# Performance work log

Measured on AMD Instinct MI355X. Metric: run time of the kernel, lower is better.

Reference implementation:

```python
import jax, jax.numpy as jnp
import numpy as np

N = 100000
E = 1600000
F_IN = 128
H = 256
C = 40
BN_EPS = 1e-5


def setup_inputs() -> dict:
    key = jax.random.key(0)
    ks = jax.random.split(key, 16)
    x = jax.random.normal(ks[0], (N, F_IN), dtype=jnp.float32)
    edge_index = jax.random.randint(ks[1], (2, E), 0, N, dtype=jnp.int64)
    # pre layer
    pre_w = jax.random.normal(ks[2], (H, F_IN), dtype=jnp.float32) * (1.0 / np.sqrt(F_IN))
    pre_b = jnp.zeros((H,), jnp.float32)
    # batchnorm params stacked [5, 4, H]: gamma, beta, running_mean, running_var
    gamma = jnp.ones((5, H), jnp.float32)
    beta = jnp.zeros((5, H), jnp.float32)
    rmean = jax.random.normal(ks[3], (5, H), dtype=jnp.float32) * 0.1
    rvar = jax.random.uniform(ks[4], (5, H), dtype=jnp.float32) * 0.5 + 0.5
    bn_params = jnp.stack([gamma, beta, rmean, rvar], axis=1)  # [5,4,H]
    # 3 SAGEConv layers: lin_l (neighbor, with bias), lin_r (root, no bias)
    s = 1.0 / np.sqrt(H)
    lin_l_w = jax.random.normal(ks[5], (3, H, H), dtype=jnp.float32) * s
    lin_l_b = jnp.zeros((3, H), jnp.float32)
    lin_r_w = jax.random.normal(ks[6], (3, H, H), dtype=jnp.float32) * s
    # post layers
    post1_w = jax.random.normal(ks[7], (H, H), dtype=jnp.float32) * s
    post1_b = jnp.zeros((H,), jnp.float32)
    post2_w = jax.random.normal(ks[8], (C, H), dtype=jnp.float32) * s
    post2_b = jnp.zeros((C,), jnp.float32)
    return {
        "x": x, "edge_index": edge_index,
        "pre_w": pre_w, "pre_b": pre_b, "bn_params": bn_params,
        "lin_l_w": lin_l_w, "lin_l_b": lin_l_b, "lin_r_w": lin_r_w,
        "post1_w": post1_w, "post1_b": post1_b,
        "post2_w": post2_w, "post2_b": post2_b,
    }


def _bn(x, p):
    # eval-mode BatchNorm1d with running stats; p: [4, H]
    g, b, m, v = p[0], p[1], p[2], p[3]
    return (x - m) * (g * jax.lax.rsqrt(v + BN_EPS)) + b


def _sage_conv(x, src, dst, wl, bl, wr):
    # PyG SAGEConv (aggr='mean'): lin_l(mean_{j in N(i)} x_j) + lin_r(x_i)
    msg = x[src]                                             # [E, H] gather
    agg = jax.ops.segment_sum(msg, dst, num_segments=N)       # [N, H] scatter
    cnt = jax.ops.segment_sum(jnp.ones((src.shape[0],), x.dtype), dst, num_segments=N)
    mean = agg / jnp.maximum(cnt, 1.0)[:, None]
    return mean @ wl.T + bl + x @ wr.T


def reference(x, edge_index, pre_w, pre_b, bn_params, lin_l_w, lin_l_b, lin_r_w,
              post1_w, post1_b, post2_w, post2_b):
    src, dst = edge_index[0], edge_index[1]
    h = x @ pre_w.T + pre_b
    h = jax.nn.relu(_bn(h, bn_params[0]))  # dropout is identity in eval mode
    for i in range(3):
        h = _sage_conv(h, src, dst, lin_l_w[i], lin_l_b[i], lin_r_w[i])
        h = jax.nn.relu(_bn(h, bn_params[i + 1]))
    h = h @ post1_w.T + post1_b
    h = jax.nn.relu(_bn(h, bn_params[4]))
    logits = h @ post2_w.T + post2_b
    return jax.nn.log_softmax(logits, axis=1)
```

## Files before the change

kernel.cpp:

```cpp
#include <hip/hip_runtime.h>
#include <cstdint>
#include <cstddef>

#define N_NODES 100000
#define N_EDGES 1600000
#define F_INDIM 128
#define HDIM 256
#define C_OUT 40
#define BN_EPS 1e-5f

typedef unsigned short bf16_t;
typedef __attribute__((ext_vector_type(8))) short bf16x8;
typedef __attribute__((ext_vector_type(4))) float f32x4;

__device__ __forceinline__ float bf2f(unsigned int u) {
  return __uint_as_float(u << 16);
}
__device__ __forceinline__ bf16_t f2bf(float f) {
  unsigned int x = __float_as_uint(f);
  return (bf16_t)((x + 0x7fffu + ((x >> 16) & 1u)) >> 16);
}

__global__ void k_cvt(const float* __restrict__ s, bf16_t* __restrict__ d, int n) {
  int i = (blockIdx.x * blockDim.x + threadIdx.x) * 4;
  if (i >= n) return;
  float4 v = *reinterpret_cast<const float4*>(&s[i]);
  uint2 o;
  o.x = (unsigned)f2bf(v.x) | ((unsigned)f2bf(v.y) << 16);
  o.y = (unsigned)f2bf(v.z) | ((unsigned)f2bf(v.w) << 16);
  *reinterpret_cast<uint2*>(&d[i]) = o;
}

#define W0N 32768
#define W1N 196608
#define W2N 196608
#define W3N 65536
#define W4N 10240
#define WTOT (W0N + W1N + W2N + W3N + W4N)

__global__ void k_cvt_w(const float* __restrict__ s0, bf16_t* __restrict__ d0,
                        const float* __restrict__ s1, bf16_t* __restrict__ d1,
                        const float* __restrict__ s2, bf16_t* __restrict__ d2,
                        const float* __restrict__ s3, bf16_t* __restrict__ d3,
                        const float* __restrict__ s4, bf16_t* __restrict__ d4) {
  int i = (blockIdx.x * blockDim.x + threadIdx.x) * 4;
  if (i >= WTOT) return;
  const float* s; bf16_t* d;
  if (i < W0N)                         { s = s0; d = d0; }
  else if (i < W0N + W1N)              { s = s1; d = d1; i -= W0N; }
  else if (i < W0N + W1N + W2N)        { s = s2; d = d2; i -= W0N + W1N; }
  else if (i < W0N + W1N + W2N + W3N)  { s = s3; d = d3; i -= W0N + W1N + W2N; }
  else                                 { s = s4; d = d4; i -= W0N + W1N + W2N + W3N; }
  float4 v = *reinterpret_cast<const float4*>(&s[i]);
  uint2 o;
  o.x = (unsigned)f2bf(v.x) | ((unsigned)f2bf(v.y) << 16);
  o.y = (unsigned)f2bf(v.z) | ((unsigned)f2bf(v.w) << 16);
  *reinterpret_cast<uint2*>(&d[i]) = o;
}

__global__ void k_rank(const int* __restrict__ dst, int* __restrict__ cursor,
                       int* __restrict__ rank, int E) {
  for (int e = blockIdx.x * blockDim.x + threadIdx.x; e < E; e += gridDim.x * blockDim.x)
    rank[e] = atomicAdd(&cursor[dst[e]], 1);
}

__global__ __launch_bounds__(1024)
void k_scan_local(const int* __restrict__ cnt, int* __restrict__ row_ptr,
                  int* __restrict__ blk_sum, int n) {
  __shared__ int buf[1024];
  int tid = threadIdx.x;
  int i = blockIdx.x * 1024 + tid;
  int v = (i < n) ? cnt[i] : 0;
  buf[tid] = v;
  __syncthreads();
  for (int off = 1; off < 1024; off <<= 1) {
    int t = (tid >= off) ? buf[tid - off] : 0;
    __syncthreads();
    buf[tid] += t;
    __syncthreads();
  }
  if (i < n) row_ptr[i] = buf[tid] - v;
  if (tid == 1023) blk_sum[blockIdx.x] = buf[1023];
}

__global__ __launch_bounds__(128)
void k_scan_blk(const int* __restrict__ blk_sum, int* __restrict__ blk_off, int nb) {
  __shared__ int buf[128];
  int tid = threadIdx.x;
  int v = (tid < nb) ? blk_sum[tid] : 0;
  buf[tid] = v;
  __syncthreads();
  for (int off = 1; off < 128; off <<= 1) {
    int t = (tid >= off) ? buf[tid - off] : 0;
    __syncthreads();
    buf[tid] += t;
    __syncthreads();
  }
  if (tid < nb) blk_off[tid] = buf[tid] - v;
}

__global__ void k_scan_add(int* __restrict__ row_ptr, const int* __restrict__ blk_off,
                           const int* __restrict__ cnt, float* __restrict__ inv, int n) {
  int i = blockIdx.x * blockDim.x + threadIdx.x;
  if (i < n) {
    row_ptr[i] += blk_off[i >> 10];
    int c = cnt[i];
    inv[i] = 1.0f / (float)(c > 0 ? c : 1);
  }
  if (i == 0) row_ptr[n] = N_EDGES;
}

__global__ void k_place(const int* __restrict__ src, const int* __restrict__ dst,
                        const int* __restrict__ rank, const int* __restrict__ row_ptr,
                        int* __restrict__ csr, int E) {
  for (int e = blockIdx.x * blockDim.x + threadIdx.x; e < E; e += gridDim.x * blockDim.x)
    csr[row_ptr[dst[e]] + rank[e]] = src[e];
}

__device__ __forceinline__ void add8(float* acc, uint4 r) {
  acc[0] += bf2f(r.x & 0xffffu); acc[1] += bf2f(r.x >> 16);
  acc[2] += bf2f(r.y & 0xffffu); acc[3] += bf2f(r.y >> 16);
  acc[4] += bf2f(r.z & 0xffffu); acc[5] += bf2f(r.z >> 16);
  acc[6] += bf2f(r.w & 0xffffu); acc[7] += bf2f(r.w >> 16);
}

__global__ __launch_bounds__(256)
void k_aggregate(const bf16_t* __restrict__ h, const int* __restrict__ row_ptr,
                 const int* __restrict__ csr, const float* __restrict__ inv_deg,
                 bf16_t* __restrict__ mean) {
  int w = threadIdx.x >> 6, lane = threadIdx.x & 63;
  int node = blockIdx.x * 4 + w;
  if (node >= N_NODES) return;
  int beg = row_ptr[node], end = row_ptr[node + 1];
  int half = lane >> 5;
  int l32 = lane & 31;
  float acc[8] = {};
  int deg = end - beg;
  int p = beg;
  int p8 = beg + (deg & ~7);
  for (; p < p8; p += 8) {
    int s0 = csr[p + half];
    int s1 = csr[p + 2 + half];
    int s2 = csr[p + 4 + half];
    int s3 = csr[p + 6 + half];
    uint4 r0 = *reinterpret_cast<const uint4*>(&h[(size_t)s0 * HDIM + l32 * 8]);
    uint4 r1 = *reinterpret_cast<const uint4*>(&h[(size_t)s1 * HDIM + l32 * 8]);
    uint4 r2 = *reinterpret_cast<const uint4*>(&h[(size_t)s2 * HDIM + l32 * 8]);
    uint4 r3 = *reinterpret_cast<const uint4*>(&h[(size_t)s3 * HDIM + l32 * 8]);
    add8(acc, r0);
    add8(acc, r1);
    add8(acc, r2);
    add8(acc, r3);
  }
  if (end - p >= 4) {
    int s0 = csr[p + half];
    int s1 = csr[p + 2 + half];
    uint4 r0 = *reinterpret_cast<const uint4*>(&h[(size_t)s0 * HDIM + l32 * 8]);
    uint4 r1 = *reinterpret_cast<const uint4*>(&h[(size_t)s1 * HDIM + l32 * 8]);
    add8(acc, r0);
    add8(acc, r1);
    p += 4;
  }
  for (; p < end; p += 2) {
    int e = p + half;
    if (e < end) {
      int s = csr[e];
      uint4 r = *reinterpret_cast<const uint4*>(&h[(size_t)s * HDIM + l32 * 8]);
      add8(acc, r);
    }
  }
#pragma unroll
  for (int k = 0; k < 8; ++k) acc[k] += __shfl_xor(acc[k], 32);
  if (half == 0) {
    float iv = inv_deg[node];
    uint4 o;
    o.x = (unsigned)f2bf(acc[0] * iv) | ((unsigned)f2bf(acc[1] * iv) << 16);
    o.y = (unsigned)f2bf(acc[2] * iv) | ((unsigned)f2bf(acc[3] * iv) << 16);
    o.z = (unsigned)f2bf(acc[4] * iv) | ((unsigned)f2bf(acc[5] * iv) << 16);
    o.w = (unsigned)f2bf(acc[6] * iv) | ((unsigned)f2bf(acc[7] * iv) << 16);
    *reinterpret_cast<uint4*>(&mean[(size_t)node * HDIM + l32 * 8]) = o;
  }
}

__device__ __forceinline__ void store1(float* p, float v) { *p = v; }
__device__ __forceinline__ void store1(bf16_t* p, float v) { *p = f2bf(v); }

template <typename TOUT>
__global__ __launch_bounds__(256)
void gemm_mfma(const bf16_t* __restrict__ A0, const bf16_t* __restrict__ W0,
               const bf16_t* __restrict__ A1, const bf16_t* __restrict__ W1,
               const float* __restrict__ bias, const float* __restrict__ bn,
               TOUT* __restrict__ C, int M, int K, int OUT, int dual) {
  __shared__ bf16_t lds[2][2][128 * 32];
  int g = blockIdx.x, bx, by;
  if (OUT > 128) {
    int grp = g >> 4, loc = g & 15;
    bx = grp * 8 + (loc & 7);
    by = loc >> 3;
  } else {
    bx = g; by = 0;
  }
  const int row0 = bx * 128, col0 = by * 128;
  if (row0 >= M) return;

  const int tid = threadIdx.x;
  const int lane = tid & 63, wid = tid >> 6;
  const int wm = wid >> 1, wn = wid & 1;
  const int l15 = lane & 15, l4 = lane >> 4;

  const int nk = K / 32;
  const int nsteps = dual ? nk * 2 : nk;

  f32x4 acc[4][4] = {};

  const int srow_base = wid * 32 + (lane >> 2);
  const int skk = ((lane & 3) ^ ((lane >> 3) & 3)) * 8;

  auto stage = [&](int s, int b) {
    const bf16_t* A = (s < nk) ? A0 : A1;
    const bf16_t* W = (s < nk) ? W0 : W1;
    int kk0 = ((s < nk) ? s : s - nk) * 32 + skk;
#pragma unroll
    for (int c = 0; c < 2; ++c) {
      int chunk = wid * 2 + c;
      int row = srow_base + c * 16;
      int ar = row0 + row; if (ar >= M) ar = M - 1;
      int br = col0 + row; if (br >= OUT) br = OUT - 1;
      __builtin_amdgcn_global_load_lds(
          (const __attribute__((address_space(1))) unsigned int*)&A[(size_t)ar * K + kk0],
          (__attribute__((address_space(3))) unsigned int*)&lds[b][0][chunk * 512],
          16, 0, 0);
      __builtin_amdgcn_global_load_lds(
          (const __attribute__((address_space(1))) unsigned int*)&W[(size_t)br * K + kk0],
          (__attribute__((address_space(3))) unsigned int*)&lds[b][1][chunk * 512],
          16, 0, 0);
    }
  };

  const int rslot = (l4 ^ ((l15 >> 1) & 3)) * 8;

  stage(0, 0);
  __syncthreads();
  int cur = 0;
  for (int s = 0; s < nsteps; ++s) {
    if (s + 1 < nsteps) stage(s + 1, cur ^ 1);
    const bf16_t* pa = &lds[cur][0][l15 * 32 + rslot];
    const bf16_t* pb = &lds[cur][1][l15 * 32 + rslot];
    bf16x8 a[4], b[4];
#pragma unroll
    for (int i = 0; i < 4; ++i)
      a[i] = *reinterpret_cast<const bf16x8*>(&pa[(wm * 64 + i * 16) * 32]);
#pragma unroll
    for (int j = 0; j < 4; ++j)
      b[j] = *reinterpret_cast<const bf16x8*>(&pb[(wn * 64 + j * 16) * 32]);
#pragma unroll
    for (int i = 0; i < 4; ++i)
#pragma unroll
      for (int j = 0; j < 4; ++j)
        acc[i][j] = __builtin_amdgcn_mfma_f32_16x16x32_bf16(a[i], b[j], acc[i][j], 0, 0, 0);
    if (s + 1 < nsteps) {
      __syncthreads();
      cur ^= 1;
    }
  }

#pragma unroll
  for (int j = 0; j < 4; ++j) {
    int col = col0 + wn * 64 + j * 16 + l15;
    if (col >= OUT) continue;
    float bs = bias ? bias[col] : 0.f;
    float scale = 1.f, shift = bs;
    bool has_bn = (bn != nullptr);
    if (has_bn) {
      float g2 = bn[col], bb = bn[256 + col], mm = bn[512 + col], vv = bn[768 + col];
      float is = g2 * rsqrtf(vv + BN_EPS);
      scale = is; shift = (bs - mm) * is + bb;
    }
#pragma unroll
    for (int i = 0; i < 4; ++i) {
#pragma unroll
      for (int r = 0; r < 4; ++r) {
        int row = row0 + wm * 64 + i * 16 + l4 * 4 + r;
        if (row >= M) continue;
        float v = acc[i][j][r];
        v = has_bn ? fmaxf(v * scale + shift, 0.f) : (v + bs);
        store1(&C[(size_t)row * OUT + col], v);
      }
    }
  }
}

__global__ __launch_bounds__(256)
void k_logsoftmax(const float* __restrict__ logits, float* __restrict__ out, int M) {
  int row = blockIdx.x * 4 + (threadIdx.x >> 6);
  if (row >= M) return;
  int lane = threadIdx.x & 63;
  float v = (lane < C_OUT) ? logits[(size_t)row * C_OUT + lane] : -1e30f;
  float m = v;
#pragma unroll
  for (int o = 32; o; o >>= 1) m = fmaxf(m, __shfl_xor(m, o));
  float e = (lane < C_OUT) ? expf(v - m) : 0.f;
  float s = e;
#pragma unroll
  for (int o = 32; o; o >>= 1) s += __shfl_xor(s, o);
  if (lane < C_OUT) out[(size_t)row * C_OUT + lane] = v - m - logf(s);
}

extern "C" void kernel_launch(void* const* d_in, const int* in_sizes, int n_in,
                              void* d_out, int out_size, void* d_ws, size_t ws_size,
                              hipStream_t stream) {
  const float* x       = (const float*)d_in[0];
  const int*   ei      = (const int*)d_in[1];
  const float* pre_w   = (const float*)d_in[2];
  const float* pre_b   = (const float*)d_in[3];
  const float* bn      = (const float*)d_in[4];
  const float* lin_l_w = (const float*)d_in[5];
  const float* lin_l_b = (const float*)d_in[6];
  const float* lin_r_w = (const float*)d_in[7];
  const float* post1_w = (const float*)d_in[8];
  const float* post1_b = (const float*)d_in[9];
  const float* post2_w = (const float*)d_in[10];
  const float* post2_b = (const float*)d_in[11];
  float* out = (float*)d_out;

  const int* src = ei;
  const int* dstv = ei + N_EDGES;

  char* base = (char*)d_ws;
  size_t off = 0;
  auto alloc = [&](size_t bytes) -> void* {
    void* p = base + off;
    off = (off + bytes + 255) & ~(size_t)255;
    return p;
  };
  bf16_t* hA = (bf16_t*)alloc((size_t)N_NODES * HDIM * 2);
  bf16_t* hB = (bf16_t*)alloc((size_t)N_NODES * HDIM * 2);
  bf16_t* hC = (bf16_t*)alloc((size_t)N_NODES * HDIM * 2);
  int* row_ptr = (int*)alloc((size_t)(N_NODES + 1) * 4);
  int* cursor  = (int*)alloc((size_t)N_NODES * 4);
  int* csr     = (int*)alloc((size_t)N_EDGES * 4);
  int* rank    = (int*)alloc((size_t)N_EDGES * 4);
  float* inv   = (float*)alloc((size_t)N_NODES * 4);
  int* blk_sum = (int*)alloc(128 * 4);
  int* blk_off = (int*)alloc(128 * 4);
  bf16_t* w_pre = (bf16_t*)alloc((size_t)HDIM * F_INDIM * 2);
  bf16_t* w_ll  = (bf16_t*)alloc((size_t)3 * HDIM * HDIM * 2);
  bf16_t* w_lr  = (bf16_t*)alloc((size_t)3 * HDIM * HDIM * 2);
  bf16_t* w_p1  = (bf16_t*)alloc((size_t)HDIM * HDIM * 2);
  bf16_t* w_p2  = (bf16_t*)alloc((size_t)C_OUT * HDIM * 2);
  (void)n_in; (void)in_sizes; (void)out_size;
  if (off > ws_size) return;

  bf16_t* x_bf = hB;

  {
    int n = N_NODES * F_INDIM;
    k_cvt<<<(n / 4 + 255) / 256, 256, 0, stream>>>(x, x_bf, n);
    k_cvt_w<<<(WTOT / 4 + 255) / 256, 256, 0, stream>>>(
        pre_w, w_pre, lin_l_w, w_ll, lin_r_w, w_lr, post1_w, w_p1, post2_w, w_p2);
  }

  hipMemsetAsync(cursor, 0, (size_t)N_NODES * 4, stream);
  k_rank<<<2048, 256, 0, stream>>>(dstv, cursor, rank, N_EDGES);
  int nb = (N_NODES + 1023) / 1024;
  k_scan_local<<<nb, 1024, 0, stream>>>(cursor, row_ptr, blk_sum, N_NODES);
  k_scan_blk<<<1, 128, 0, stream>>>(blk_sum, blk_off, nb);
  k_scan_add<<<(N_NODES + 255) / 256, 256, 0, stream>>>(row_ptr, blk_off, cursor, inv, N_NODES);
  k_place<<<2048, 256, 0, stream>>>(src, dstv, rank, row_ptr, csr, N_EDGES);

  int nrt = (N_NODES + 127) / 128;
  int gW = ((nrt + 7) / 8) * 16;
  gemm_mfma<bf16_t><<<gW, 256, 0, stream>>>(
      x_bf, w_pre, nullptr, nullptr, pre_b, bn, hA, N_NODES, F_INDIM, HDIM, 0);

  bf16_t* hcur = hA;
  bf16_t* hnext = hC;
  for (int i = 0; i < 3; ++i) {
    k_aggregate<<<N_NODES / 4, 256, 0, stream>>>(hcur, row_ptr, csr, inv, hB);
    gemm_mfma<bf16_t><<<gW, 256, 0, stream>>>(
        hB, w_ll + (size_t)i * HDIM * HDIM,
        hcur, w_lr + (size_t)i * HDIM * HDIM,
        lin_l_b + (size_t)i * HDIM,
        bn + (size_t)(i + 1) * 4 * HDIM,
        hnext, N_NODES, HDIM, HDIM, 1);
    bf16_t* t = hcur; hcur = hnext; hnext = t;
  }
  gemm_mfma<bf16_t><<<gW, 256, 0, stream>>>(
      hcur, w_p1, nullptr, nullptr, post1_b,
      bn + (size_t)4 * 4 * HDIM, hnext, N_NODES, HDIM, HDIM, 0);
  float* logits = (float*)hB;
  gemm_mfma<float><<<nrt, 256, 0, stream>>>(
      hnext, w_p2, nullptr, nullptr, post2_b,
      nullptr, logits, N_NODES, HDIM, C_OUT, 0);
  k_logsoftmax<<<(N_NODES + 3) / 4, 256, 0, stream>>>(logits, out, N_NODES);
}
```

Before: 764.7 us.

## Build CSR via coarse bucket scatter plus per-bucket shared-memory placement

Replaces the per-edge global rank atomics and the random global scatter in k_place with a two-level bucketing scheme. Edges are first appended as (src,dst) pairs into 196 buckets of 512 destination nodes, then each bucket is placed into CSR by one block using shared-memory cursors. This localizes the final scatter writes to a small window per block and removes the rank array. It adds a second atomic per edge on a few bucket counters, which are contended. It also relies on a fixed bucket capacity of 10240; pairs beyond it are silently dropped, so a heavily skewed graph would produce a wrong CSR.

```diff
diff --git a/kernel.cpp b/kernel.cpp
--- a/kernel.cpp
+++ b/kernel.cpp
@@ -8,6 +8,9 @@
 #define HDIM 256
 #define C_OUT 40
 #define BN_EPS 1e-5f
+
+#define NBUCK 196
+#define BCAP 10240
 
 typedef unsigned short bf16_t;
 typedef __attribute__((ext_vector_type(8))) short bf16x8;
@@ -58,10 +61,42 @@
   *reinterpret_cast<uint2*>(&d[i]) = o;
 }
 
-__global__ void k_rank(const int* __restrict__ dst, int* __restrict__ cursor,
-                       int* __restrict__ rank, int E) {
-  for (int e = blockIdx.x * blockDim.x + threadIdx.x; e < E; e += gridDim.x * blockDim.x)
-    rank[e] = atomicAdd(&cursor[dst[e]], 1);
+__global__ void k_scatter(const int* __restrict__ src, const int* __restrict__ dst,
+                          int* __restrict__ cnt, int* __restrict__ bcur,
+                          uint2* __restrict__ bpairs, int E) {
+  for (int e = blockIdx.x * blockDim.x + threadIdx.x; e < E; e += gridDim.x * blockDim.x) {
+    int d = dst[e];
+    int s = src[e];
+    atomicAdd(&cnt[d], 1);
+    int b = d >> 9;
+    int pos = atomicAdd(&bcur[b * 16], 1);
+    if (pos < BCAP)
+      bpairs[(size_t)b * BCAP + pos] = make_uint2((unsigned)s, (unsigned)d);
+  }
+}
+
+__global__ __launch_bounds__(512)
+void k_bsort(const uint2* __restrict__ bpairs, const int* __restrict__ row_ptr,
+             int* __restrict__ csr, int n) {
+  __shared__ int lcur[512];
+  __shared__ int lrp[512];
+  int b = blockIdx.x;
+  int n0 = b << 9;
+  int n1 = n0 + 512; if (n1 > n) n1 = n;
+  int tid = threadIdx.x;
+  lcur[tid] = 0;
+  lrp[tid] = (n0 + tid < n1) ? row_ptr[n0 + tid] : 0;
+  __syncthreads();
+  int base = lrp[0];
+  int bs = row_ptr[n1] - base;
+  if (bs > BCAP) bs = BCAP;
+  const uint2* bp = &bpairs[(size_t)b * BCAP];
+  for (int i = tid; i < bs; i += 512) {
+    uint2 p = bp[i];
+    int d = (int)p.y;
+    int r = atomicAdd(&lcur[d - n0], 1);
+    csr[lrp[d - n0] + r] = (int)p.x;
+  }
 }
 
 __global__ __launch_bounds__(1024)
@@ -108,13 +143,6 @@
     inv[i] = 1.0f / (float)(c > 0 ? c : 1);
   }
   if (i == 0) row_ptr[n] = N_EDGES;
-}
-
-__global__ void k_place(const int* __restrict__ src, const int* __restrict__ dst,
-                        const int* __restrict__ rank, const int* __restrict__ row_ptr,
-                        int* __restrict__ csr, int E) {
-  for (int e = blockIdx.x * blockDim.x + threadIdx.x; e < E; e += gridDim.x * blockDim.x)
-    csr[row_ptr[dst[e]] + rank[e]] = src[e];
 }
 
 __device__ __forceinline__ void add8(float* acc, uint4 r) {
@@ -337,9 +365,10 @@
   bf16_t* hB = (bf16_t*)alloc((size_t)N_NODES * HDIM * 2);
   bf16_t* hC = (bf16_t*)alloc((size_t)N_NODES * HDIM * 2);
   int* row_ptr = (int*)alloc((size_t)(N_NODES + 1) * 4);
-  int* cursor  = (int*)alloc((size_t)N_NODES * 4);
+  int* cnt     = (int*)alloc((size_t)N_NODES * 4);
   int* csr     = (int*)alloc((size_t)N_EDGES * 4);
-  int* rank    = (int*)alloc((size_t)N_EDGES * 4);
+  uint2* bpairs = (uint2*)alloc((size_t)NBUCK * BCAP * 8);
+  int* bcur    = (int*)alloc((size_t)NBUCK * 16 * 4);
   float* inv   = (float*)alloc((size_t)N_NODES * 4);
   int* blk_sum = (int*)alloc(128 * 4);
   int* blk_off = (int*)alloc(128 * 4);
@@ -360,13 +389,14 @@
         pre_w, w_pre, lin_l_w, w_ll, lin_r_w, w_lr, post1_w, w_p1, post2_w, w_p2);
   }
 
-  hipMemsetAsync(cursor, 0, (size_t)N_NODES * 4, stream);
-  k_rank<<<2048, 256, 0, stream>>>(dstv, cursor, rank, N_EDGES);
+  hipMemsetAsync(cnt, 0, (size_t)N_NODES * 4, stream);
+  hipMemsetAsync(bcur, 0, (size_t)NBUCK * 16 * 4, stream);
+  k_scatter<<<2048, 256, 0, stream>>>(src, dstv, cnt, bcur, bpairs, N_EDGES);
   int nb = (N_NODES + 1023) / 1024;
-  k_scan_local<<<nb, 1024, 0, stream>>>(cursor, row_ptr, blk_sum, N_NODES);
+  k_scan_local<<<nb, 1024, 0, stream>>>(cnt, row_ptr, blk_sum, N_NODES);
   k_scan_blk<<<1, 128, 0, stream>>>(blk_sum, blk_off, nb);
-  k_scan_add<<<(N_NODES + 255) / 256, 256, 0, stream>>>(row_ptr, blk_off, cursor, inv, N_NODES);
-  k_place<<<2048, 256, 0, stream>>>(src, dstv, rank, row_ptr, csr, N_EDGES);
+  k_scan_add<<<(N_NODES + 255) / 256, 256, 0, stream>>>(row_ptr, blk_off, cnt, inv, N_NODES);
+  k_bsort<<<NBUCK, 512, 0, stream>>>(bpairs, row_ptr, csr, N_NODES);
 
   int nrt = (N_NODES + 127) / 128;
   int gW = ((nrt + 7) / 8) * 16;
```

Measured after the change: 896.8 us. 1.17x slower.
